# Performance work log

Measured on AMD Instinct MI355X. Metric: run time of the kernel, lower is better.

## Reference

```python
import jax, jax.numpy as jnp
import numpy as np

B, N, C_FEAT, FH, FW = 2, 6, 128, 28, 60
D, HEADS, DHEAD = 128, 4, 32
BH, BW = 32, 32
IMG_H, IMG_W = 224, 480
EPS = 1e-5

def _generate_grid(h, w):
    xs = np.linspace(0.0, 1.0, w, dtype=np.float32)
    ys = np.linspace(0.0, 1.0, h, dtype=np.float32)
    gx, gy = np.meshgrid(xs, ys, indexing='xy')  # (h, w)
    return np.stack([gx, gy, np.ones_like(gx)], 0)  # (3, h, w) homogeneous

def setup_inputs():
    key = jax.random.key(0)
    ks = iter(jax.random.split(key, 64))
    def nrm(shape, s=0.02):
        return jax.random.normal(next(ks), shape, dtype=jnp.float32) * s
    inp = {}
    inp['x'] = jax.random.normal(next(ks), (B, D, BH, BW), jnp.float32)
    inp['feature'] = jax.random.normal(next(ks), (B, N, C_FEAT, FH, FW), jnp.float32)
    inp['I_inv'] = jax.random.normal(next(ks), (B, N, 3, 3), jnp.float32)
    inp['E_inv'] = jax.random.normal(next(ks), (B, N, 4, 4), jnp.float32)
    inp['bev_grid'] = jax.random.uniform(next(ks), (3, BH, BW), jnp.float32) * 100.0
    plane = _generate_grid(FH, FW)
    plane[0] *= IMG_W
    plane[1] *= IMG_H
    inp['image_plane'] = jnp.asarray(plane)
    # feature_linear (fl) and feature_proj (fp): BN (eval) -> ReLU -> 1x1 conv
    for p in ('fl', 'fp'):
        inp[p + '_bn_g'] = jnp.ones((C_FEAT,), jnp.float32)
        inp[p + '_bn_b'] = jnp.zeros((C_FEAT,), jnp.float32)
        inp[p + '_bn_m'] = nrm((C_FEAT,), 0.1)
        inp[p + '_bn_v'] = jnp.ones((C_FEAT,), jnp.float32)
        inp[p + '_w'] = nrm((D, C_FEAT))
    inp['bev_w'] = nrm((D, 2)); inp['bev_b'] = nrm((D,))
    inp['img_w'] = nrm((D, 4)); inp['cam_w'] = nrm((D, 4))
    md = HEADS * DHEAD
    for p in ('q', 'k', 'v'):
        inp[p + '_ln_g'] = jnp.ones((D,), jnp.float32)
        inp[p + '_ln_b'] = jnp.zeros((D,), jnp.float32)
        inp[p + '_w'] = nrm((D, md))
        inp[p + '_b'] = nrm((md,))
    inp['proj_w'] = nrm((md, D)); inp['proj_b'] = nrm((D,))
    inp['pre_g'] = jnp.ones((D,), jnp.float32); inp['pre_b'] = jnp.zeros((D,), jnp.float32)
    inp['mlp_w1'] = nrm((D, 2 * D)); inp['mlp_b1'] = nrm((2 * D,))
    inp['mlp_w2'] = nrm((2 * D, D)); inp['mlp_b2'] = nrm((D,))
    inp['post_g'] = jnp.ones((D,), jnp.float32); inp['post_b'] = jnp.zeros((D,), jnp.float32)
    return inp

def _ln(t, g, b):
    mu = jnp.mean(t, -1, keepdims=True)
    var = jnp.mean((t - mu) ** 2, -1, keepdims=True)
    return (t - mu) * jax.lax.rsqrt(var + EPS) * g + b

def _bn_relu_conv(t, g, b, m, v, w):
    # eval-mode BatchNorm2d -> ReLU -> 1x1 conv (no bias); t: (B, C, H, W)
    th = (t - m[:, None, None]) * (g / jnp.sqrt(v + EPS))[:, None, None] + b[:, None, None]
    return jnp.einsum('oc,bchw->bohw', w, jax.nn.relu(th))

def reference(x, feature, I_inv, E_inv, bev_grid, image_plane,
              fl_bn_g, fl_bn_b, fl_bn_m, fl_bn_v, fl_w,
              fp_bn_g, fp_bn_b, fp_bn_m, fp_bn_v, fp_w,
              bev_w, bev_b, img_w, cam_w,
              q_ln_g, q_ln_b, q_w, q_b,
              k_ln_g, k_ln_b, k_w, k_b,
              v_ln_g, v_ln_b, v_w, v_b,
              proj_w, proj_b, pre_g, pre_b,
              mlp_w1, mlp_b1, mlp_w2, mlp_b2, post_g, post_b):
    b, n = feature.shape[:2]
    h, w = image_plane.shape[-2:]
    H, W = x.shape[-2:]
    dm = x.shape[1]
    # camera-center embedding: cam_embed 1x1 conv on translation column of E_inv
    c = E_inv[..., -1]                                             # (b, n, 4)
    c_embed = jnp.einsum('oc,bnc->bno', cam_w, c).reshape(b * n, dm)
    # per-pixel ray directions in world frame: d = E_inv @ pad(I_inv @ pixel, 1)
    pix = image_plane.reshape(3, h * w)
    cam = jnp.einsum('bnij,jk->bnik', I_inv, pix)                  # (b, n, 3, hw)
    cam = jnp.concatenate([cam, jnp.ones((b, n, 1, h * w), cam.dtype)], 2)
    d = jnp.einsum('bnij,bnjk->bnik', E_inv, cam)                  # (b, n, 4, hw)
    d_embed = jnp.einsum('oc,bnck->bnok', img_w, d).reshape(b * n, dm, h, w)
    img_embed = d_embed - c_embed[:, :, None, None]
    img_embed = img_embed / (jnp.linalg.norm(img_embed, axis=1, keepdims=True) + 1e-7)
    # bev positional embedding: bev_embed conv1x1 on world xy, minus camera embed
    w_embed = jnp.einsum('oc,chw->ohw', bev_w, bev_grid[:2]) + bev_b[:, None, None]
    bev_embed = w_embed[None] - c_embed[:, :, None, None]          # (bn, d, H, W)
    bev_embed = bev_embed / (jnp.linalg.norm(bev_embed, axis=1, keepdims=True) + 1e-7)
    query_pos = bev_embed.reshape(b, n, dm, H, W)
    feat_flat = feature.reshape(b * n, feature.shape[2], h, w)
    key_flat = img_embed + _bn_relu_conv(feat_flat, fp_bn_g, fp_bn_b, fp_bn_m, fp_bn_v, fp_w)
    val_flat = _bn_relu_conv(feat_flat, fl_bn_g, fl_bn_b, fl_bn_m, fl_bn_v, fl_w)
    query = query_pos + x[:, None]                                 # (b, n, d, H, W)
    # --- cross attention (softmax over all cameras' keys jointly) ---
    Q, K = H * W, h * w
    q = query.reshape(b, n, dm, Q).transpose(0, 1, 3, 2)           # (b, n, Q, d)
    k = key_flat.reshape(b, n, dm, K).transpose(0, 1, 3, 2)        # (b, n, K, d)
    v = val_flat.reshape(b, n, dm, K).transpose(0, 1, 3, 2).reshape(b, n * K, dm)
    q = _ln(q, q_ln_g, q_ln_b) @ q_w + q_b
    k = _ln(k, k_ln_g, k_ln_b) @ k_w + k_b
    v = _ln(v, v_ln_g, v_ln_b) @ v_w + v_b
    m, dh = HEADS, DHEAD
    qh = q.reshape(b, n, Q, m, dh)
    kh = k.reshape(b, n, K, m, dh)
    vh = v.reshape(b, n * K, m, dh)
    dot = (dh ** -0.5) * jnp.einsum('bnqmd,bnkmd->bmqnk', qh, kh)  # (b,m,Q,n,K)
    att = jax.nn.softmax(dot.reshape(b, m, Q, n * K), axis=-1)
    a = jnp.einsum('bmqK,bKmd->bqmd', att, vh).reshape(b, Q, m * dh)
    z = a @ proj_w + proj_b
    z = z + x.reshape(b, dm, Q).transpose(0, 2, 1)                 # skip connection
    z = _ln(z, pre_g, pre_b)
    z = z + (jax.nn.gelu(z @ mlp_w1 + mlp_b1, approximate=False) @ mlp_w2 + mlp_b2)
    z = _ln(z, post_g, post_b)
    return z.transpose(0, 2, 1).reshape(b, dm, H, W)
```

## Files before the change

### kernel.cpp

```cpp
#include <hip/hip_runtime.h>
#include <math.h>

#define EPSF 1e-5f

#define BB 2
#define NN 6
#define KPIX 1680
#define QQ 1024
#define SPLIT 6
#define KCHUNK (KPIX/SPLIT)
#define NPART (NN*SPLIT)
#define QKSCALE (0.17677669529663687f * 1.4426950408889634f)
#define NTILE_KV 53
#define KVGRID (BB*NN*NTILE_KV)

#define WOFF_FP   0
#define WOFF_FL   16384
#define WOFF_K    32768
#define WOFF_V    49152
#define WOFF_Q    65536
#define WOFF_PROJ 81920
#define WOFF_W1   98304
#define WOFF_W2   131072
#define WPK_ELEMS 163840

typedef __attribute__((ext_vector_type(8))) short bf16x8;
typedef __attribute__((ext_vector_type(16))) float f32x16;

__device__ __forceinline__ unsigned short f2bf(float f) {
  union { float f; unsigned u; } v; v.f = f;
  unsigned r = v.u + 0x7FFFu + ((v.u >> 16) & 1u);
  return (unsigned short)(r >> 16);
}
__device__ __forceinline__ float bf2f(unsigned short u) {
  union { unsigned u; float f; } v; v.u = ((unsigned)u) << 16; return v.f;
}
__device__ __forceinline__ unsigned pk_bf16(float lo, float hi) {
  unsigned r;
  asm volatile("v_cvt_pk_bf16_f32 %0, %1, %2" : "=v"(r) : "v"(lo), "v"(hi));
  return r;
}
__device__ __forceinline__ float fast_exp2(float x) {
  return __builtin_amdgcn_exp2f(x);
}
__device__ __forceinline__ void half_swap(unsigned &a, unsigned &b) {
#if __has_builtin(__builtin_amdgcn_permlane32_swap)
  auto r = __builtin_amdgcn_permlane32_swap(a, b, false, false);
  a = (unsigned)r[0]; b = (unsigned)r[1];
#else
  unsigned sa = (unsigned)__shfl_xor((int)a, 32);
  unsigned sb = (unsigned)__shfl_xor((int)b, 32);
  int hi = (threadIdx.x & 63) >> 5;
  unsigned na = hi ? sb : a;
  unsigned nb = hi ? b : sa;
  a = na; b = nb;
#endif
}

__global__ void pre_kernel(const float* __restrict__ fp_w, const float* __restrict__ fl_w,
                           const float* __restrict__ k_w, const float* __restrict__ v_w,
                           const float* __restrict__ q_w, const float* __restrict__ proj_w,
                           const float* __restrict__ mlp_w1, const float* __restrict__ mlp_w2,
                           const float* __restrict__ cam_w, const float* __restrict__ E_inv,
                           unsigned short* __restrict__ wp, float* __restrict__ c_embed) {
  int blk = blockIdx.x;
  int c = threadIdx.x;
  if (blk < 640) {
    int mat = blk >> 7, o = blk & 127;
    float v;
    if (mat == 0)      v = fp_w[o*128 + c];
    else if (mat == 1) v = fl_w[o*128 + c];
    else if (mat == 2) v = k_w[c*128 + o];
    else if (mat == 3) v = v_w[c*128 + o];
    else               v = q_w[c*128 + o] * QKSCALE;
    wp[(size_t)mat*16384 + o*128 + c] = f2bf(v);
  } else if (blk < 768) {
    int row = blk - 640;
    wp[WOFF_PROJ + row*128 + c] = f2bf(proj_w[c*128 + row]);
  } else if (blk < 1024) {
    int row = blk - 768;
    wp[WOFF_W1 + row*128 + c] = f2bf(mlp_w1[c*256 + row]);
  } else if (blk < 1280) {
    int i2 = blk - 1024;
    int row = i2 >> 1, col = (i2 & 1)*128 + c;
    wp[WOFF_W2 + row*256 + col] = f2bf(mlp_w2[col*128 + row]);
  } else {
    int bn = blk - 1280;
    const float* E = E_inv + bn * 16;
    float s = cam_w[c*4+0]*E[3] + cam_w[c*4+1]*E[7] + cam_w[c*4+2]*E[11] + cam_w[c*4+3]*E[15];
    c_embed[bn*128 + c] = s;
  }
}

__global__ __launch_bounds__(256) void proj_kernel(
    const float* __restrict__ feature, const float* __restrict__ I_inv,
    const float* __restrict__ E_inv, const float* __restrict__ image_plane,
    const float* __restrict__ c_embed, const float* __restrict__ img_w,
    const float* __restrict__ fp_bn_g, const float* __restrict__ fp_bn_b,
    const float* __restrict__ fp_bn_m, const float* __restrict__ fp_bn_v,
    const float* __restrict__ fl_bn_g, const float* __restrict__ fl_bn_b,
    const float* __restrict__ fl_bn_m, const float* __restrict__ fl_bn_v,
    const float* __restrict__ k_ln_g, const float* __restrict__ k_ln_b,
    const float* __restrict__ k_b,
    const float* __restrict__ v_ln_g, const float* __restrict__ v_ln_b,
    const float* __restrict__ v_b,
    const float* __restrict__ x, const float* __restrict__ bev_grid,
    const float* __restrict__ bev_w, const float* __restrict__ bev_b,
    const float* __restrict__ q_ln_g, const float* __restrict__ q_ln_b,
    const float* __restrict__ q_b,
    const unsigned short* __restrict__ wp,
    unsigned short* __restrict__ khb, unsigned short* __restrict__ vtb,
    unsigned short* __restrict__ qhb)
{
  __shared__ __align__(16) unsigned char smem[19456];
  int t = threadIdx.x;

  if (blockIdx.x < KVGRID) {
    unsigned short (*sA)[32*128] = reinterpret_cast<unsigned short(*)[32*128]>(smem);
    float (*sD)[32]     = reinterpret_cast<float(*)[32]>(smem + 16384);
    float (*sRed)[4][32] = reinterpret_cast<float(*)[4][32]>(smem + 16384 + 512);

    int blk = blockIdx.x;
    int bn = blk / NTILE_KV, tp = blk % NTILE_KV;
    int p0 = tp * 32;
    int wv = t >> 6, l = t & 63, lo = l & 31, hi = l >> 5;

    if (t < 32) {
      int pix = min(p0 + t, KPIX-1);
      const float* Ii = I_inv + bn*9;
      const float* Ei = E_inv + bn*16;
      float px = image_plane[pix], py = image_plane[KPIX + pix], pz = image_plane[2*KPIX + pix];
      float c0 = Ii[0]*px + Ii[1]*py + Ii[2]*pz;
      float c1 = Ii[3]*px + Ii[4]*py + Ii[5]*pz;
      float c2 = Ii[6]*px + Ii[7]*py + Ii[8]*pz;
      sD[0][t] = Ei[0]*c0 + Ei[1]*c1 + Ei[2]*c2  + Ei[3];
      sD[1][t] = Ei[4]*c0 + Ei[5]*c1 + Ei[6]*c2  + Ei[7];
      sD[2][t] = Ei[8]*c0 + Ei[9]*c1 + Ei[10]*c2 + Ei[11];
      sD[3][t] = Ei[12]*c0 + Ei[13]*c1 + Ei[14]*c2 + Ei[15];
    }

    {
      int path = t >> 7;
      int cp = (t >> 1) & 63;
      int ph = t & 1;
      int c0 = cp * 2;
      const float* bg = path ? fl_bn_g : fp_bn_g;
      const float* bb = path ? fl_bn_b : fp_bn_b;
      const float* bm = path ? fl_bn_m : fp_bn_m;
      const float* bv = path ? fl_bn_v : fp_bn_v;
      float g0 = bg[c0+0]*rsqrtf(bv[c0+0]+EPSF); float o0 = bb[c0+0] - bm[c0+0]*g0;
      float g1 = bg[c0+1]*rsqrtf(bv[c0+1]+EPSF); float o1 = bb[c0+1] - bm[c0+1]*g1;
      const float* frow0 = feature + ((size_t)bn*128 + c0)*KPIX;
      const float* frow1 = frow0 + KPIX;
#pragma unroll
      for (int i = 0; i < 4; ++i) {
        int plb = ph*16 + 4*i;
        int pix = p0 + plb;
        float4 f0, f1;
        if (pix + 3 < KPIX) {
          f0 = *(const float4*)(frow0 + pix);
          f1 = *(const float4*)(frow1 + pix);
        } else {
          f0.x = frow0[min(pix+0, KPIX-1)]; f0.y = frow0[min(pix+1, KPIX-1)];
          f0.z = frow0[min(pix+2, KPIX-1)]; f0.w = frow0[min(pix+3, KPIX-1)];
          f1.x = frow1[min(pix+0, KPIX-1)]; f1.y = frow1[min(pix+1, KPIX-1)];
          f1.z = frow1[min(pix+2, KPIX-1)]; f1.w = frow1[min(pix+3, KPIX-1)];
        }
        float fa[4] = {f0.x, f0.y, f0.z, f0.w};
        float fb[4] = {f1.x, f1.y, f1.z, f1.w};
#pragma unroll
        for (int j = 0; j < 4; ++j) {
          int pl = plb + j;
          int cc = c0 ^ ((pl & 7) << 3);
          ushort2 w;
          w.x = f2bf(fmaxf(fa[j]*g0 + o0, 0.f));
          w.y = f2bf(fmaxf(fb[j]*g1 + o1, 0.f));
          *(ushort2*)&sA[path][pl*128 + cc] = w;
        }
      }
    }
    __syncthreads();

    f32x16 acck = {}, accv = {};
    {
      const unsigned short* wfp = wp + WOFF_FP + (32*wv + lo)*128 + hi*8;
      const unsigned short* wfl = wp + WOFF_FL + (32*wv + lo)*128 + hi*8;
      int swz = (lo & 7) << 3;
#pragma unroll
      for (int s = 0; s < 8; ++s) {
        int cbase = s*16 + hi*8;
        bf16x8 a0 = *(const bf16x8*)(wfp + s*16);
        bf16x8 a1 = *(const bf16x8*)(wfl + s*16);
        bf16x8 b0 = *(const bf16x8*)&sA[0][lo*128 + (cbase ^ swz)];
        bf16x8 b1 = *(const bf16x8*)&sA[1][lo*128 + (cbase ^ swz)];
        acck = __builtin_amdgcn_mfma_f32_32x32x16_bf16(a0, b0, acck, 0, 0, 0);
        accv = __builtin_amdgcn_mfma_f32_32x32x16_bf16(a1, b1, accv, 0, 0, 0);
      }
    }

    float d0 = sD[0][lo], d1 = sD[1][lo], d2 = sD[2][lo], d3 = sD[3][lo];

    float ime[16];
    float ss = 0.f, vs1 = 0.f, vs2 = 0.f;
#pragma unroll
    for (int r = 0; r < 16; ++r) {
      int o = 32*wv + (r&3) + 8*(r>>2) + 4*hi;
      float4 iw = *(const float4*)(img_w + o*4);
      float de = iw.x*d0 + iw.y*d1 + iw.z*d2 + iw.w*d3 - c_embed[bn*128 + o];
      ime[r] = de; ss += de*de;
      float vv = accv[r];
      vs1 += vv; vs2 += vv*vv;
    }
    ss  += __shfl_xor(ss, 32);
    vs1 += __shfl_xor(vs1, 32);
    vs2 += __shfl_xor(vs2, 32);
    if (hi == 0) { sRed[0][wv][lo] = ss; sRed[1][wv][lo] = vs1; sRed[2][wv][lo] = vs2; }
    __syncthreads();
    float sst  = sRed[0][0][lo]+sRed[0][1][lo]+sRed[0][2][lo]+sRed[0][3][lo];
    float vs1t = sRed[1][0][lo]+sRed[1][1][lo]+sRed[1][2][lo]+sRed[1][3][lo];
    float vs2t = sRed[2][0][lo]+sRed[2][1][lo]+sRed[2][2][lo]+sRed[2][3][lo];
    float rinv = 1.f/(sqrtf(sst) + 1e-7f);
    float vmu = vs1t*(1.f/128.f);
    float vrs = rsqrtf(vs2t*(1.f/128.f) - vmu*vmu + EPSF);

    float kval[16];
    float ks1 = 0.f, ks2 = 0.f;
#pragma unroll
    for (int r = 0; r < 16; ++r) {
      float kv2 = acck[r] + ime[r]*rinv;
      kval[r] = kv2; ks1 += kv2; ks2 += kv2*kv2;
    }
    ks1 += __shfl_xor(ks1, 32);
    ks2 += __shfl_xor(ks2, 32);
    if (hi == 0) { sRed[3][wv][lo] = ks1; sRed[4][wv][lo] = ks2; }
    __syncthreads();
    float ks1t = sRed[3][0][lo]+sRed[3][1][lo]+sRed[3][2][lo]+sRed[3][3][lo];
    float ks2t = sRed[4][0][lo]+sRed[4][1][lo]+sRed[4][2][lo]+sRed[4][3][lo];
    float kmu = ks1t*(1.f/128.f);
    float krs = rsqrtf(ks2t*(1.f/128.f) - kmu*kmu + EPSF);

    {
      int swz = (lo & 7) << 3;
#pragma unroll
      for (int g = 0; g < 4; ++g) {
        int ob = 32*wv + 8*g + 4*hi;
        float4 kg = *(const float4*)(k_ln_g + ob);
        float4 kb2 = *(const float4*)(k_ln_b + ob);
        float4 vg = *(const float4*)(v_ln_g + ob);
        float4 vb2 = *(const float4*)(v_ln_b + ob);
        float kn0 = (kval[4*g+0]-kmu)*krs*kg.x + kb2.x;
        float kn1 = (kval[4*g+1]-kmu)*krs*kg.y + kb2.y;
        float kn2 = (kval[4*g+2]-kmu)*krs*kg.z + kb2.z;
        float kn3 = (kval[4*g+3]-kmu)*krs*kg.w + kb2.w;
        float vn0 = (accv[4*g+0]-vmu)*vrs*vg.x + vb2.x;
        float vn1 = (accv[4*g+1]-vmu)*vrs*vg.y + vb2.y;
        float vn2 = (accv[4*g+2]-vmu)*vrs*vg.z + vb2.z;
        float vn3 = (accv[4*g+3]-vmu)*vrs*vg.w + vb2.w;
        int idx = lo*128 + (ob ^ swz);
        *(ushort4*)&sA[0][idx] = make_ushort4(f2bf(kn0), f2bf(kn1), f2bf(kn2), f2bf(kn3));
        *(ushort4*)&sA[1][idx] = make_ushort4(f2bf(vn0), f2bf(vn1), f2bf(vn2), f2bf(vn3));
      }
    }
    __syncthreads();

    f32x16 a2k = {}, a2v = {};
    {
      const unsigned short* wk = wp + WOFF_K + (32*wv + lo)*128 + hi*8;
      const unsigned short* wv2 = wp + WOFF_V + (32*wv + lo)*128 + hi*8;
      int swz = (lo & 7) << 3;
#pragma unroll
      for (int s = 0; s < 8; ++s) {
        int cbase = s*16 + hi*8;
        bf16x8 a0 = *(const bf16x8*)(wk + s*16);
        bf16x8 a1 = *(const bf16x8*)(wv2 + s*16);
        bf16x8 b0 = *(const bf16x8*)&sA[0][lo*128 + (cbase ^ swz)];
        bf16x8 b1 = *(const bf16x8*)&sA[1][lo*128 + (cbase ^ swz)];
        a2k = __builtin_amdgcn_mfma_f32_32x32x16_bf16(a0, b0, a2k, 0, 0, 0);
        a2v = __builtin_amdgcn_mfma_f32_32x32x16_bf16(a1, b1, a2v, 0, 0, 0);
      }
    }

    int pix = p0 + lo;
    if (pix < KPIX) {
      unsigned short* krow = khb + ((size_t)bn*KPIX + pix)*128;
#pragma unroll
      for (int g = 0; g < 4; ++g) {
        int ob = 32*wv + 8*g + 4*hi;
        float4 kb4 = *(const float4*)(k_b + ob);
        *(ushort4*)(krow + ob) = make_ushort4(
          f2bf(a2k[4*g+0] + kb4.x), f2bf(a2k[4*g+1] + kb4.y),
          f2bf(a2k[4*g+2] + kb4.z), f2bf(a2k[4*g+3] + kb4.w));
        float4 vb4 = *(const float4*)(v_b + ob);
        vtb[((size_t)bn*128 + ob+0)*KPIX + pix] = f2bf(a2v[4*g+0] + vb4.x);
        vtb[((size_t)bn*128 + ob+1)*KPIX + pix] = f2bf(a2v[4*g+1] + vb4.y);
        vtb[((size_t)bn*128 + ob+2)*KPIX + pix] = f2bf(a2v[4*g+2] + vb4.z);
        vtb[((size_t)bn*128 + ob+3)*KPIX + pix] = f2bf(a2v[4*g+3] + vb4.w);
      }
    }
  } else {
    unsigned short* sQ = reinterpret_cast<unsigned short*>(smem);
    float (*sRedQ)[8][32] = reinterpret_cast<float(*)[8][32]>(smem + 8192);

    int qblk = blockIdx.x - KVGRID;
    int bn = qblk >> 5, qt = qblk & 31;
    int p0 = qt * 32;
    int b = bn / NN;

    {
      int q = t & 31, og = t >> 5;
      int qi = p0 + q;
      float gx = bev_grid[qi], gy = bev_grid[QQ + qi];
      float be[16]; float ss = 0.f;
#pragma unroll
      for (int j = 0; j < 16; ++j) {
        int o = og*16 + j;
        float we = bev_w[o*2+0]*gx + bev_w[o*2+1]*gy + bev_b[o];
        float v = we - c_embed[bn*128 + o];
        be[j] = v; ss += v*v;
      }
      sRedQ[0][og][q] = ss;
      __syncthreads();
      float sst = 0.f;
#pragma unroll
      for (int g = 0; g < 8; ++g) sst += sRedQ[0][g][q];
      float rinv = 1.f/(sqrtf(sst) + 1e-7f);
      float s1 = 0.f, s2 = 0.f;
#pragma unroll
      for (int j = 0; j < 16; ++j) {
        int o = og*16 + j;
        float qv = be[j]*rinv + x[((size_t)(b*128 + o))*QQ + qi];
        be[j] = qv; s1 += qv; s2 += qv*qv;
      }
      sRedQ[1][og][q] = s1; sRedQ[2][og][q] = s2;
      __syncthreads();
      float s1t = 0.f, s2t = 0.f;
#pragma unroll
      for (int g = 0; g < 8; ++g) { s1t += sRedQ[1][g][q]; s2t += sRedQ[2][g][q]; }
      float mu = s1t*(1.f/128.f);
      float rs = rsqrtf(s2t*(1.f/128.f) - mu*mu + EPSF);
      int swz = (q & 7) << 3;
#pragma unroll
      for (int u = 0; u < 4; ++u) {
        int ob = og*16 + 4*u;
        float4 qg = *(const float4*)(q_ln_g + ob);
        float4 qb2 = *(const float4*)(q_ln_b + ob);
        *(ushort4*)&sQ[q*128 + (ob ^ swz)] = make_ushort4(
          f2bf((be[4*u+0]-mu)*rs*qg.x + qb2.x), f2bf((be[4*u+1]-mu)*rs*qg.y + qb2.y),
          f2bf((be[4*u+2]-mu)*rs*qg.z + qb2.z), f2bf((be[4*u+3]-mu)*rs*qg.w + qb2.w));
      }
    }
    __syncthreads();

    {
      int wvv = t >> 6, l = t & 63, lo = l & 31, hi = l >> 5;
      const unsigned short* wq = wp + WOFF_Q + (32*wvv + lo)*128 + hi*8;
      int swz = (lo & 7) << 3;
      f32x16 acc = {};
#pragma unroll
      for (int s = 0; s < 8; ++s) {
        int cbase = s*16 + hi*8;
        bf16x8 a0 = *(const bf16x8*)(wq + s*16);
        bf16x8 b0 = *(const bf16x8*)&sQ[lo*128 + (cbase ^ swz)];
        acc = __builtin_amdgcn_mfma_f32_32x32x16_bf16(a0, b0, acc, 0, 0, 0);
      }
      unsigned short* qrow = qhb + ((size_t)bn*QQ + p0 + lo)*128;
#pragma unroll
      for (int g = 0; g < 4; ++g) {
        int ob = 32*wvv + 8*g + 4*hi;
        float4 qb4 = *(const float4*)(q_b + ob);
        *(ushort4*)(qrow + ob) = make_ushort4(
          f2bf(acc[4*g+0] + qb4.x*QKSCALE), f2bf(acc[4*g+1] + qb4.y*QKSCALE),
          f2bf(acc[4*g+2] + qb4.z*QKSCALE), f2bf(acc[4*g+3] + qb4.w*QKSCALE));
      }
    }
  }
}

__global__ __launch_bounds__(256) void attn_kernel(
    const unsigned short* __restrict__ qhb, const unsigned short* __restrict__ khb,
    const unsigned short* __restrict__ vtb,
    float* __restrict__ lsum, unsigned short* __restrict__ pacb)
{
  int blk = blockIdx.x;
  int sp = blk % SPLIT; blk /= SPLIT;
  int n  = blk % NN;    blk /= NN;
  int qt = blk % 16;    blk /= 16;
  int b  = blk;
  int t = threadIdx.x;
  int wave = t >> 6, l = t & 63, lo = l & 31, hi = l >> 5;
  int dho = wave * 32;
  int bn = b*NN + n;

  bf16x8 qf[2][2];
#pragma unroll
  for (int g = 0; g < 2; ++g) {
    const unsigned short* qrow = qhb + ((size_t)bn*QQ + qt*64 + g*32 + lo)*128 + dho + hi*8;
    qf[g][0] = *(const bf16x8*)(qrow);
    qf[g][1] = *(const bf16x8*)(qrow + 16);
  }

  f32x16 acc[2] = {};
  float lr[2] = {0.f, 0.f};

  int k0 = sp * KCHUNK, kend = k0 + KCHUNK;
  int kfull_end = k0 + (KCHUNK & ~31);
  const unsigned short* kbase = khb + (size_t)bn*KPIX*128 + dho + hi*8;
  const unsigned short* vrow  = vtb + ((size_t)bn*128 + dho + lo)*KPIX;

  bf16x8 kf0, kf1, vf0, vf1;
  {
    const unsigned short* krow = kbase + (size_t)(k0 + lo)*128;
    kf0 = *(const bf16x8*)(krow);
    kf1 = *(const bf16x8*)(krow + 16);
    vf0 = *(const bf16x8*)(vrow + k0 + hi*8);
    vf1 = *(const bf16x8*)(vrow + k0 + 16 + hi*8);
  }

  for (int K0 = k0; K0 < kfull_end; K0 += 32) {
    int Kn = K0 + 32;
    const unsigned short* krow = kbase + (size_t)(Kn + lo)*128;
    bf16x8 nk0 = *(const bf16x8*)(krow);
    bf16x8 nk1 = *(const bf16x8*)(krow + 16);
    bf16x8 nv0 = *(const bf16x8*)(vrow + Kn + hi*8);
    bf16x8 nv1 = *(const bf16x8*)(vrow + Kn + 16 + hi*8);

#pragma unroll
    for (int g = 0; g < 2; ++g) {
      f32x16 s = {};
      __builtin_amdgcn_s_setprio(1);
      s = __builtin_amdgcn_mfma_f32_32x32x16_bf16(kf0, qf[g][0], s, 0, 0, 0);
      s = __builtin_amdgcn_mfma_f32_32x32x16_bf16(kf1, qf[g][1], s, 0, 0, 0);
      __builtin_amdgcn_s_setprio(0);
      float p[16];
      float lsub = 0.f;
#pragma unroll
      for (int r = 0; r < 16; ++r) { float e = fast_exp2(s[r]); p[r] = e; lsub += e; }
      lr[g] += lsub;
#pragma unroll
      for (int ks = 0; ks < 2; ++ks) {
        int rb = ks*8;
        unsigned a0 = pk_bf16(p[rb+0], p[rb+1]);
        unsigned c0 = pk_bf16(p[rb+2], p[rb+3]);
        unsigned b0 = pk_bf16(p[rb+4], p[rb+5]);
        unsigned d0 = pk_bf16(p[rb+6], p[rb+7]);
        half_swap(a0, b0);
        half_swap(c0, d0);
        union { unsigned u[4]; bf16x8 v; } pa;
        pa.u[0] = a0; pa.u[1] = c0; pa.u[2] = b0; pa.u[3] = d0;
        __builtin_amdgcn_s_setprio(1);
        acc[g] = __builtin_amdgcn_mfma_f32_32x32x16_bf16(pa.v, ks ? vf1 : vf0, acc[g], 0, 0, 0);
        __builtin_amdgcn_s_setprio(0);
      }
    }
    kf0 = nk0; kf1 = nk1; vf0 = nv0; vf1 = nv1;
  }

  {
    int K0 = kfull_end;
#pragma unroll
    for (int g = 0; g < 2; ++g) {
      f32x16 s = {};
      __builtin_amdgcn_s_setprio(1);
      s = __builtin_amdgcn_mfma_f32_32x32x16_bf16(kf0, qf[g][0], s, 0, 0, 0);
      s = __builtin_amdgcn_mfma_f32_32x32x16_bf16(kf1, qf[g][1], s, 0, 0, 0);
      __builtin_amdgcn_s_setprio(0);
      float p[16];
      float lsub = 0.f;
#pragma unroll
      for (int r = 0; r < 16; ++r) {
        int key = K0 + (r&3) + 8*(r>>2) + 4*hi;
        float e = (key < kend) ? fast_exp2(s[r]) : 0.f;
        p[r] = e; lsub += e;
      }
      lr[g] += lsub;
#pragma unroll
      for (int ks = 0; ks < 2; ++ks) {
        int rb = ks*8;
        unsigned a0 = pk_bf16(p[rb+0], p[rb+1]);
        unsigned c0 = pk_bf16(p[rb+2], p[rb+3]);
        unsigned b0 = pk_bf16(p[rb+4], p[rb+5]);
        unsigned d0 = pk_bf16(p[rb+6], p[rb+7]);
        half_swap(a0, b0);
        half_swap(c0, d0);
        union { unsigned u[4]; bf16x8 v; } pa;
        pa.u[0] = a0; pa.u[1] = c0; pa.u[2] = b0; pa.u[3] = d0;
        __builtin_amdgcn_s_setprio(1);
        acc[g] = __builtin_amdgcn_mfma_f32_32x32x16_bf16(pa.v, ks ? vf1 : vf0, acc[g], 0, 0, 0);
        __builtin_amdgcn_s_setprio(0);
      }
    }
  }

  size_t hb = ((size_t)(b*4 + wave)*NPART + (n*SPLIT + sp))*QQ;
#pragma unroll
  for (int g = 0; g < 2; ++g) {
    float ltot = lr[g] + __shfl_xor(lr[g], 32);
    if (hi == 0) lsum[hb + qt*64 + g*32 + lo] = ltot;
#pragma unroll
    for (int r = 0; r < 16; ++r) {
      int crow = (r&3) + 8*(r>>2) + 4*hi;
      pacb[(hb + qt*64 + g*32 + crow)*32 + lo] = f2bf(acc[g][r]);
    }
  }
}

__global__ __launch_bounds__(512) void epi_kernel(
    const float* __restrict__ lsum, const unsigned short* __restrict__ pacb,
    const float* __restrict__ x, const unsigned short* __restrict__ wp,
    const float* __restrict__ proj_b,
    const float* __restrict__ pre_g, const float* __restrict__ pre_b,
    const float* __restrict__ mlp_b1, const float* __restrict__ mlp_b2,
    const float* __restrict__ post_g, const float* __restrict__ post_b,
    float* __restrict__ out)
{
  int blk = blockIdx.x;
  int b = blk >> 5, qt = blk & 31;
  int q0 = qt * 32;
  int t = threadIdx.x;
  int wv = t >> 6, l = t & 63, lo = l & 31, hi = l >> 5;
  int rt = wv & 3, kh = wv >> 2;

  __shared__ unsigned short sA[32*128];
  __shared__ unsigned short sZ[32*128];
  __shared__ unsigned short sH[32*256];
  __shared__ float sPar[4][64][16];
  __shared__ float sRedE[2][4][32];

  {
    int q = t & 31, g = t >> 5;
    int m = g >> 2, dl = (g & 3) * 8;
    size_t basehm = ((size_t)(b*4 + m)*NPART)*QQ + q0 + q;
    float lt = 0.f;
    float av[8] = {0,0,0,0,0,0,0,0};
    for (int j = 0; j < NPART; ++j) {
      size_t base = basehm + (size_t)j*QQ;
      lt += lsum[base];
      const unsigned short* pp = pacb + base*32 + dl;
      ushort4 u0 = *(const ushort4*)(pp);
      ushort4 u1 = *(const ushort4*)(pp + 4);
      av[0] += bf2f(u0.x); av[1] += bf2f(u0.y); av[2] += bf2f(u0.z); av[3] += bf2f(u0.w);
      av[4] += bf2f(u1.x); av[5] += bf2f(u1.y); av[6] += bf2f(u1.z); av[7] += bf2f(u1.w);
    }
    float rl = 1.f / lt;
    int swz = (q & 7) << 3;
    int dg = (g*8) ^ swz;
    *(ushort4*)&sA[q*128 + dg] = make_ushort4(
      f2bf(av[0]*rl), f2bf(av[1]*rl), f2bf(av[2]*rl), f2bf(av[3]*rl));
    *(ushort4*)&sA[q*128 + dg + 4] = make_ushort4(
      f2bf(av[4]*rl), f2bf(av[5]*rl), f2bf(av[6]*rl), f2bf(av[7]*rl));
  }
  __syncthreads();

  f32x16 acc = {};
  {
    const unsigned short* wA = wp + WOFF_PROJ + (32*rt + lo)*128 + kh*64 + hi*8;
    int swz = (lo & 7) << 3;
#pragma unroll
    for (int s = 0; s < 4; ++s) {
      int cb = kh*64 + s*16 + hi*8;
      bf16x8 a0 = *(const bf16x8*)(wA + s*16);
      bf16x8 b0 = *(const bf16x8*)&sA[lo*128 + (cb ^ swz)];
      acc = __builtin_amdgcn_mfma_f32_32x32x16_bf16(a0, b0, acc, 0, 0, 0);
    }
  }
  if (wv >= 4) {
#pragma unroll
    for (int r = 0; r < 16; ++r) sPar[wv-4][l][r] = acc[r];
  }
  __syncthreads();

  float znr[16], zv[16];
  if (wv < 4) {
    float s1 = 0.f, s2 = 0.f;
#pragma unroll
    for (int r = 0; r < 16; ++r) {
      int o = 32*rt + (r&3) + 8*(r>>2) + 4*hi;
      float z = acc[r] + sPar[wv][l][r] + proj_b[o] + x[((size_t)b*128 + o)*QQ + q0 + lo];
      zv[r] = z; s1 += z; s2 += z*z;
    }
    s1 += __shfl_xor(s1, 32); s2 += __shfl_xor(s2, 32);
    if (hi == 0) { sRedE[0][rt][lo] = s1; sRedE[1][rt][lo] = s2; }
  }
  __syncthreads();
  if (wv < 4) {
    float s1t = sRedE[0][0][lo]+sRedE[0][1][lo]+sRedE[0][2][lo]+sRedE[0][3][lo];
    float s2t = sRedE[1][0][lo]+sRedE[1][1][lo]+sRedE[1][2][lo]+sRedE[1][3][lo];
    float mu = s1t*(1.f/128.f);
    float rs = rsqrtf(s2t*(1.f/128.f) - mu*mu + EPSF);
    int swz = (lo & 7) << 3;
#pragma unroll
    for (int g2 = 0; g2 < 4; ++g2) {
      int ob = 32*rt + 8*g2 + 4*hi;
      float4 pg = *(const float4*)(pre_g + ob);
      float4 pb = *(const float4*)(pre_b + ob);
      float z0 = (zv[4*g2+0]-mu)*rs*pg.x + pb.x;
      float z1 = (zv[4*g2+1]-mu)*rs*pg.y + pb.y;
      float z2 = (zv[4*g2+2]-mu)*rs*pg.z + pb.z;
      float z3 = (zv[4*g2+3]-mu)*rs*pg.w + pb.w;
      znr[4*g2+0] = z0; znr[4*g2+1] = z1; znr[4*g2+2] = z2; znr[4*g2+3] = z3;
      *(ushort4*)&sZ[lo*128 + (ob ^ swz)] = make_ushort4(f2bf(z0), f2bf(z1), f2bf(z2), f2bf(z3));
    }
  }
  __syncthreads();

  {
    f32x16 acch = {};
    const unsigned short* wA = wp + WOFF_W1 + (32*wv + lo)*128 + hi*8;
    int swz = (lo & 7) << 3;
#pragma unroll
    for (int s = 0; s < 8; ++s) {
      int cb = s*16 + hi*8;
      bf16x8 a0 = *(const bf16x8*)(wA + s*16);
      bf16x8 b0 = *(const bf16x8*)&sZ[lo*128 + (cb ^ swz)];
      acch = __builtin_amdgcn_mfma_f32_32x32x16_bf16(a0, b0, acch, 0, 0, 0);
    }
#pragma unroll
    for (int g2 = 0; g2 < 4; ++g2) {
      int hrow = 32*wv + 8*g2 + 4*hi;
      float4 b1 = *(const float4*)(mlp_b1 + hrow);
      float h0 = acch[4*g2+0] + b1.x, h1 = acch[4*g2+1] + b1.y;
      float h2 = acch[4*g2+2] + b1.z, h3 = acch[4*g2+3] + b1.w;
      float g0 = 0.5f*h0*(1.f + erff(h0*0.7071067811865476f));
      float g1 = 0.5f*h1*(1.f + erff(h1*0.7071067811865476f));
      float g2f = 0.5f*h2*(1.f + erff(h2*0.7071067811865476f));
      float g3 = 0.5f*h3*(1.f + erff(h3*0.7071067811865476f));
      *(ushort4*)&sH[lo*256 + (hrow ^ swz)] = make_ushort4(f2bf(g0), f2bf(g1), f2bf(g2f), f2bf(g3));
    }
  }
  __syncthreads();

  f32x16 acc2 = {};
  {
    const unsigned short* wA = wp + WOFF_W2 + (32*rt + lo)*256 + kh*128 + hi*8;
    int swz = (lo & 7) << 3;
#pragma unroll
    for (int s = 0; s < 8; ++s) {
      int cb = kh*128 + s*16 + hi*8;
      bf16x8 a0 = *(const bf16x8*)(wA + s*16);
      bf16x8 b0 = *(const bf16x8*)&sH[lo*256 + (cb ^ swz)];
      acc2 = __builtin_amdgcn_mfma_f32_32x32x16_bf16(a0, b0, acc2, 0, 0, 0);
    }
  }
  if (wv >= 4) {
#pragma unroll
    for (int r = 0; r < 16; ++r) sPar[wv-4][l][r] = acc2[r];
  }
  __syncthreads();

  float z2v[16];
  if (wv < 4) {
    float s1 = 0.f, s2 = 0.f;
#pragma unroll
    for (int r = 0; r < 16; ++r) {
      int o = 32*rt + (r&3) + 8*(r>>2) + 4*hi;
      float z2 = znr[r] + acc2[r] + sPar[wv][l][r] + mlp_b2[o];
      z2v[r] = z2; s1 += z2; s2 += z2*z2;
    }
    s1 += __shfl_xor(s1, 32); s2 += __shfl_xor(s2, 32);
    if (hi == 0) { sRedE[0][rt][lo] = s1; sRedE[1][rt][lo] = s2; }
  }
  __syncthreads();
  if (wv < 4) {
    float s1t = sRedE[0][0][lo]+sRedE[0][1][lo]+sRedE[0][2][lo]+sRedE[0][3][lo];
    float s2t = sRedE[1][0][lo]+sRedE[1][1][lo]+sRedE[1][2][lo]+sRedE[1][3][lo];
    float mu = s1t*(1.f/128.f);
    float rs = rsqrtf(s2t*(1.f/128.f) - mu*mu + EPSF);
#pragma unroll
    for (int r = 0; r < 16; ++r) {
      int o = 32*rt + (r&3) + 8*(r>>2) + 4*hi;
      out[((size_t)b*128 + o)*QQ + q0 + lo] = (z2v[r]-mu)*rs*post_g[o] + post_b[o];
    }
  }
}

extern "C" void kernel_launch(void* const* d_in, const int* in_sizes, int n_in,
                              void* d_out, int out_size, void* d_ws, size_t ws_size,
                              hipStream_t stream) {
  const float* x           = (const float*)d_in[0];
  const float* feature     = (const float*)d_in[1];
  const float* I_inv       = (const float*)d_in[2];
  const float* E_inv       = (const float*)d_in[3];
  const float* bev_grid    = (const float*)d_in[4];
  const float* image_plane = (const float*)d_in[5];
  const float* fl_bn_g = (const float*)d_in[6];
  const float* fl_bn_b = (const float*)d_in[7];
  const float* fl_bn_m = (const float*)d_in[8];
  const float* fl_bn_v = (const float*)d_in[9];
  const float* fl_w    = (const float*)d_in[10];
  const float* fp_bn_g = (const float*)d_in[11];
  const float* fp_bn_b = (const float*)d_in[12];
  const float* fp_bn_m = (const float*)d_in[13];
  const float* fp_bn_v = (const float*)d_in[14];
  const float* fp_w    = (const float*)d_in[15];
  const float* bev_w   = (const float*)d_in[16];
  const float* bev_b   = (const float*)d_in[17];
  const float* img_w   = (const float*)d_in[18];
  const float* cam_w   = (const float*)d_in[19];
  const float* q_ln_g  = (const float*)d_in[20];
  const float* q_ln_b  = (const float*)d_in[21];
  const float* q_w     = (const float*)d_in[22];
  const float* q_b     = (const float*)d_in[23];
  const float* k_ln_g  = (const float*)d_in[24];
  const float* k_ln_b  = (const float*)d_in[25];
  const float* k_w     = (const float*)d_in[26];
  const float* k_b     = (const float*)d_in[27];
  const float* v_ln_g  = (const float*)d_in[28];
  const float* v_ln_b  = (const float*)d_in[29];
  const float* v_w     = (const float*)d_in[30];
  const float* v_b     = (const float*)d_in[31];
  const float* proj_w  = (const float*)d_in[32];
  const float* proj_b  = (const float*)d_in[33];
  const float* pre_g   = (const float*)d_in[34];
  const float* pre_b   = (const float*)d_in[35];
  const float* mlp_w1  = (const float*)d_in[36];
  const float* mlp_b1  = (const float*)d_in[37];
  const float* mlp_w2  = (const float*)d_in[38];
  const float* mlp_b2  = (const float*)d_in[39];
  const float* post_g  = (const float*)d_in[40];
  const float* post_b  = (const float*)d_in[41];

  float* ws = (float*)d_ws;
  float* c_embed = ws;
  float* lsum = ws + 1536;
  unsigned short* pacb = (unsigned short*)(lsum + (size_t)BB*4*NPART*QQ);
  unsigned short* qhb = pacb + (size_t)BB*4*NPART*QQ*32;
  unsigned short* khb = qhb + (size_t)BB*NN*QQ*128;
  unsigned short* vtb = khb + (size_t)BB*NN*KPIX*128;
  unsigned short* wpk = vtb + (size_t)BB*NN*KPIX*128;
  float* out = (float*)d_out;

  hipLaunchKernelGGL(pre_kernel, dim3(1280 + BB*NN), dim3(128), 0, stream,
                     fp_w, fl_w, k_w, v_w, q_w, proj_w, mlp_w1, mlp_w2,
                     cam_w, E_inv, wpk, c_embed);
  hipLaunchKernelGGL(proj_kernel, dim3(KVGRID + BB*NN*32), dim3(256), 0, stream,
                     feature, I_inv, E_inv, image_plane, c_embed, img_w,
                     fp_bn_g, fp_bn_b, fp_bn_m, fp_bn_v,
                     fl_bn_g, fl_bn_b, fl_bn_m, fl_bn_v,
                     k_ln_g, k_ln_b, k_b,
                     v_ln_g, v_ln_b, v_b,
                     x, bev_grid, bev_w, bev_b,
                     q_ln_g, q_ln_b, q_b,
                     wpk, khb, vtb, qhb);
  hipLaunchKernelGGL(attn_kernel, dim3(BB*16*NN*SPLIT), dim3(256), 0, stream,
                     qhb, khb, vtb, lsum, pacb);
  hipLaunchKernelGGL(epi_kernel, dim3(BB*32), dim3(512), 0, stream,
                     lsum, pacb, x, wpk, proj_b, pre_g, pre_b,
                     mlp_b1, mlp_b2, post_g, post_b, out);
}
```

Measured before the change: 87.45 us.

## Fully unroll attention key loop in pairs and precompute KV embed norm before sync

The attention kernel's key loop now handles two 32-key tiles per step. Their QK MFMAs are interleaved, the loop is fully unrolled over the fixed chunk length of 280 keys, and the next 64 keys are prefetched. This adds instruction-level parallelism and removes loop overhead. The KV projection kernel now computes the image-embedding squared norm per pixel across all threads before the first barrier, which removes one __syncthreads and one reduction round. The cost is more register pressure from the doubled fragments, plus redundant recomputation of the camera-direction math in every thread.

```diff
diff --git a/kernel.cpp b/kernel.cpp
--- a/kernel.cpp
+++ b/kernel.cpp
@@ -112,13 +112,14 @@
     unsigned short* __restrict__ khb, unsigned short* __restrict__ vtb,
     unsigned short* __restrict__ qhb)
 {
-  __shared__ __align__(16) unsigned char smem[19456];
+  __shared__ __align__(16) unsigned char smem[19968];
   int t = threadIdx.x;
 
   if (blockIdx.x < KVGRID) {
     unsigned short (*sA)[32*128] = reinterpret_cast<unsigned short(*)[32*128]>(smem);
-    float (*sD)[32]     = reinterpret_cast<float(*)[32]>(smem + 16384);
+    float (*sD)[32]      = reinterpret_cast<float(*)[32]>(smem + 16384);
     float (*sRed)[4][32] = reinterpret_cast<float(*)[4][32]>(smem + 16384 + 512);
+    float (*sSS)[32]     = reinterpret_cast<float(*)[32]>(smem + 16384 + 512 + 2048);
 
     int blk = blockIdx.x;
     int bn = blk / NTILE_KV, tp = blk % NTILE_KV;
@@ -179,6 +180,30 @@
         }
       }
     }
+
+    {
+      int pxl = t & 31, og = t >> 5;
+      int pix = min(p0 + pxl, KPIX-1);
+      const float* Ii = I_inv + bn*9;
+      const float* Ei = E_inv + bn*16;
+      float px = image_plane[pix], py = image_plane[KPIX + pix], pz = image_plane[2*KPIX + pix];
+      float c0 = Ii[0]*px + Ii[1]*py + Ii[2]*pz;
+      float c1 = Ii[3]*px + Ii[4]*py + Ii[5]*pz;
+      float c2 = Ii[6]*px + Ii[7]*py + Ii[8]*pz;
+      float d0 = Ei[0]*c0 + Ei[1]*c1 + Ei[2]*c2  + Ei[3];
+      float d1 = Ei[4]*c0 + Ei[5]*c1 + Ei[6]*c2  + Ei[7];
+      float d2 = Ei[8]*c0 + Ei[9]*c1 + Ei[10]*c2 + Ei[11];
+      float d3 = Ei[12]*c0 + Ei[13]*c1 + Ei[14]*c2 + Ei[15];
+      float ssp = 0.f;
+#pragma unroll
+      for (int j = 0; j < 16; ++j) {
+        int o = og*16 + j;
+        float4 iw = *(const float4*)(img_w + o*4);
+        float de = iw.x*d0 + iw.y*d1 + iw.z*d2 + iw.w*d3 - c_embed[bn*128 + o];
+        ssp += de*de;
+      }
+      sSS[og][pxl] = ssp;
+    }
     __syncthreads();
 
     f32x16 acck = {}, accv = {};
@@ -198,46 +223,37 @@
       }
     }
 
+    float sst = sSS[0][lo]+sSS[1][lo]+sSS[2][lo]+sSS[3][lo]
+              + sSS[4][lo]+sSS[5][lo]+sSS[6][lo]+sSS[7][lo];
+    float rinv = 1.f/(sqrtf(sst) + 1e-7f);
     float d0 = sD[0][lo], d1 = sD[1][lo], d2 = sD[2][lo], d3 = sD[3][lo];
 
-    float ime[16];
-    float ss = 0.f, vs1 = 0.f, vs2 = 0.f;
+    float kval[16];
+    float ks1 = 0.f, ks2 = 0.f, vs1 = 0.f, vs2 = 0.f;
 #pragma unroll
     for (int r = 0; r < 16; ++r) {
       int o = 32*wv + (r&3) + 8*(r>>2) + 4*hi;
       float4 iw = *(const float4*)(img_w + o*4);
       float de = iw.x*d0 + iw.y*d1 + iw.z*d2 + iw.w*d3 - c_embed[bn*128 + o];
-      ime[r] = de; ss += de*de;
-      float vv = accv[r];
-      vs1 += vv; vs2 += vv*vv;
-    }
-    ss  += __shfl_xor(ss, 32);
-    vs1 += __shfl_xor(vs1, 32);
-    vs2 += __shfl_xor(vs2, 32);
-    if (hi == 0) { sRed[0][wv][lo] = ss; sRed[1][wv][lo] = vs1; sRed[2][wv][lo] = vs2; }
+      float kv2 = acck[r] + de*rinv;
+      kval[r] = kv2; ks1 += kv2; ks2 += kv2*kv2;
+      float vv = accv[r]; vs1 += vv; vs2 += vv*vv;
+    }
+    ks1 += __shfl_xor(ks1, 32); ks2 += __shfl_xor(ks2, 32);
+    vs1 += __shfl_xor(vs1, 32); vs2 += __shfl_xor(vs2, 32);
+    if (hi == 0) {
+      sRed[0][wv][lo] = ks1; sRed[1][wv][lo] = ks2;
+      sRed[2][wv][lo] = vs1; sRed[3][wv][lo] = vs2;
+    }
     __syncthreads();
-    float sst  = sRed[0][0][lo]+sRed[0][1][lo]+sRed[0][2][lo]+sRed[0][3][lo];
-    float vs1t = sRed[1][0][lo]+sRed[1][1][lo]+sRed[1][2][lo]+sRed[1][3][lo];
-    float vs2t = sRed[2][0][lo]+sRed[2][1][lo]+sRed[2][2][lo]+sRed[2][3][lo];
-    float rinv = 1.f/(sqrtf(sst) + 1e-7f);
+    float ks1t = sRed[0][0][lo]+sRed[0][1][lo]+sRed[0][2][lo]+sRed[0][3][lo];
+    float ks2t = sRed[1][0][lo]+sRed[1][1][lo]+sRed[1][2][lo]+sRed[1][3][lo];
+    float vs1t = sRed[2][0][lo]+sRed[2][1][lo]+sRed[2][2][lo]+sRed[2][3][lo];
+    float vs2t = sRed[3][0][lo]+sRed[3][1][lo]+sRed[3][2][lo]+sRed[3][3][lo];
+    float kmu = ks1t*(1.f/128.f);
+    float krs = rsqrtf(ks2t*(1.f/128.f) - kmu*kmu + EPSF);
     float vmu = vs1t*(1.f/128.f);
     float vrs = rsqrtf(vs2t*(1.f/128.f) - vmu*vmu + EPSF);
-
-    float kval[16];
-    float ks1 = 0.f, ks2 = 0.f;
-#pragma unroll
-    for (int r = 0; r < 16; ++r) {
-      float kv2 = acck[r] + ime[r]*rinv;
-      kval[r] = kv2; ks1 += kv2; ks2 += kv2*kv2;
-    }
-    ks1 += __shfl_xor(ks1, 32);
-    ks2 += __shfl_xor(ks2, 32);
-    if (hi == 0) { sRed[3][wv][lo] = ks1; sRed[4][wv][lo] = ks2; }
-    __syncthreads();
-    float ks1t = sRed[3][0][lo]+sRed[3][1][lo]+sRed[3][2][lo]+sRed[3][3][lo];
-    float ks2t = sRed[4][0][lo]+sRed[4][1][lo]+sRed[4][2][lo]+sRed[4][3][lo];
-    float kmu = ks1t*(1.f/128.f);
-    float krs = rsqrtf(ks2t*(1.f/128.f) - kmu*kmu + EPSF);
 
     {
       int swz = (lo & 7) << 3;
@@ -403,38 +419,111 @@
   float lr[2] = {0.f, 0.f};
 
   int k0 = sp * KCHUNK, kend = k0 + KCHUNK;
-  int kfull_end = k0 + (KCHUNK & ~31);
   const unsigned short* kbase = khb + (size_t)bn*KPIX*128 + dho + hi*8;
   const unsigned short* vrow  = vtb + ((size_t)bn*128 + dho + lo)*KPIX;
 
-  bf16x8 kf0, kf1, vf0, vf1;
+  bf16x8 kA0, kA1, vA0, vA1, kB0, kB1, vB0, vB1;
   {
-    const unsigned short* krow = kbase + (size_t)(k0 + lo)*128;
-    kf0 = *(const bf16x8*)(krow);
-    kf1 = *(const bf16x8*)(krow + 16);
-    vf0 = *(const bf16x8*)(vrow + k0 + hi*8);
-    vf1 = *(const bf16x8*)(vrow + k0 + 16 + hi*8);
-  }
-
-  for (int K0 = k0; K0 < kfull_end; K0 += 32) {
-    int Kn = K0 + 32;
-    const unsigned short* krow = kbase + (size_t)(Kn + lo)*128;
-    bf16x8 nk0 = *(const bf16x8*)(krow);
-    bf16x8 nk1 = *(const bf16x8*)(krow + 16);
-    bf16x8 nv0 = *(const bf16x8*)(vrow + Kn + hi*8);
-    bf16x8 nv1 = *(const bf16x8*)(vrow + Kn + 16 + hi*8);
-
+    const unsigned short* kr = kbase + (size_t)(k0 + lo)*128;
+    kA0 = *(const bf16x8*)(kr); kA1 = *(const bf16x8*)(kr + 16);
+    vA0 = *(const bf16x8*)(vrow + k0 + hi*8);
+    vA1 = *(const bf16x8*)(vrow + k0 + 16 + hi*8);
+    kr = kbase + (size_t)(k0 + 32 + lo)*128;
+    kB0 = *(const bf16x8*)(kr); kB1 = *(const bf16x8*)(kr + 16);
+    vB0 = *(const bf16x8*)(vrow + k0 + 32 + hi*8);
+    vB1 = *(const bf16x8*)(vrow + k0 + 32 + 16 + hi*8);
+  }
+
+#pragma unroll
+  for (int it = 0; it < 4; ++it) {
+    int K0 = k0 + it*64;
+    bf16x8 nA0, nA1, nvA0, nvA1, nB0, nB1, nvB0, nvB1;
+    {
+      int Kn = K0 + 64;
+      const unsigned short* kr = kbase + (size_t)(Kn + lo)*128;
+      nA0 = *(const bf16x8*)(kr); nA1 = *(const bf16x8*)(kr + 16);
+      nvA0 = *(const bf16x8*)(vrow + Kn + hi*8);
+      nvA1 = *(const bf16x8*)(vrow + Kn + 16 + hi*8);
+      if (it < 3) {
+        kr = kbase + (size_t)(Kn + 32 + lo)*128;
+        nB0 = *(const bf16x8*)(kr); nB1 = *(const bf16x8*)(kr + 16);
+        nvB0 = *(const bf16x8*)(vrow + Kn + 32 + hi*8);
+        nvB1 = *(const bf16x8*)(vrow + Kn + 32 + 16 + hi*8);
+      } else {
+        nB0 = nA0; nB1 = nA1; nvB0 = nvA0; nvB1 = nvA1;
+      }
+    }
+
+#pragma unroll
+    for (int g = 0; g < 2; ++g) {
+      f32x16 sA_ = {}, sB_ = {};
+      __builtin_amdgcn_s_setprio(1);
+      sA_ = __builtin_amdgcn_mfma_f32_32x32x16_bf16(kA0, qf[g][0], sA_, 0, 0, 0);
+      sB_ = __builtin_amdgcn_mfma_f32_32x32x16_bf16(kB0, qf[g][0], sB_, 0, 0, 0);
+      sA_ = __builtin_amdgcn_mfma_f32_32x32x16_bf16(kA1, qf[g][1], sA_, 0, 0, 0);
+      sB_ = __builtin_amdgcn_mfma_f32_32x32x16_bf16(kB1, qf[g][1], sB_, 0, 0, 0);
+      __builtin_amdgcn_s_setprio(0);
+      float pA[16], pB[16];
+      float lsub = 0.f;
+#pragma unroll
+      for (int r = 0; r < 16; ++r) {
+        float eA = fast_exp2(sA_[r]); pA[r] = eA;
+        float eB = fast_exp2(sB_[r]); pB[r] = eB;
+        lsub += eA + eB;
+      }
+      lr[g] += lsub;
+#pragma unroll
+      for (int ks = 0; ks < 2; ++ks) {
+        int rb = ks*8;
+        unsigned a0 = pk_bf16(pA[rb+0], pA[rb+1]);
+        unsigned c0 = pk_bf16(pA[rb+2], pA[rb+3]);
+        unsigned b0 = pk_bf16(pA[rb+4], pA[rb+5]);
+        unsigned d0 = pk_bf16(pA[rb+6], pA[rb+7]);
+        half_swap(a0, b0);
+        half_swap(c0, d0);
+        union { unsigned u[4]; bf16x8 v; } pa;
+        pa.u[0] = a0; pa.u[1] = c0; pa.u[2] = b0; pa.u[3] = d0;
+        __builtin_amdgcn_s_setprio(1);
+        acc[g] = __builtin_amdgcn_mfma_f32_32x32x16_bf16(pa.v, ks ? vA1 : vA0, acc[g], 0, 0, 0);
+        __builtin_amdgcn_s_setprio(0);
+      }
+#pragma unroll
+      for (int ks = 0; ks < 2; ++ks) {
+        int rb = ks*8;
+        unsigned a0 = pk_bf16(pB[rb+0], pB[rb+1]);
+        unsigned c0 = pk_bf16(pB[rb+2], pB[rb+3]);
+        unsigned b0 = pk_bf16(pB[rb+4], pB[rb+5]);
+        unsigned d0 = pk_bf16(pB[rb+6], pB[rb+7]);
+        half_swap(a0, b0);
+        half_swap(c0, d0);
+        union { unsigned u[4]; bf16x8 v; } pa;
+        pa.u[0] = a0; pa.u[1] = c0; pa.u[2] = b0; pa.u[3] = d0;
+        __builtin_amdgcn_s_setprio(1);
+        acc[g] = __builtin_amdgcn_mfma_f32_32x32x16_bf16(pa.v, ks ? vB1 : vB0, acc[g], 0, 0, 0);
+        __builtin_amdgcn_s_setprio(0);
+      }
+    }
+    kA0 = nA0; kA1 = nA1; vA0 = nvA0; vA1 = nvA1;
+    kB0 = nB0; kB1 = nB1; vB0 = nvB0; vB1 = nvB1;
+  }
+
+  {
+    int K0 = k0 + 256;
 #pragma unroll
     for (int g = 0; g < 2; ++g) {
       f32x16 s = {};
       __builtin_amdgcn_s_setprio(1);
-      s = __builtin_amdgcn_mfma_f32_32x32x16_bf16(kf0, qf[g][0], s, 0, 0, 0);
-      s = __builtin_amdgcn_mfma_f32_32x32x16_bf16(kf1, qf[g][1], s, 0, 0, 0);
+      s = __builtin_amdgcn_mfma_f32_32x32x16_bf16(kA0, qf[g][0], s, 0, 0, 0);
+      s = __builtin_amdgcn_mfma_f32_32x32x16_bf16(kA1, qf[g][1], s, 0, 0, 0);
       __builtin_amdgcn_s_setprio(0);
       float p[16];
       float lsub = 0.f;
 #pragma unroll
-      for (int r = 0; r < 16; ++r) { float e = fast_exp2(s[r]); p[r] = e; lsub += e; }
+      for (int r = 0; r < 16; ++r) {
+        int key = K0 + (r&3) + 8*(r>>2) + 4*hi;
+        float e = (key < kend) ? fast_exp2(s[r]) : 0.f;
+        p[r] = e; lsub += e;
+      }
       lr[g] += lsub;
 #pragma unroll
       for (int ks = 0; ks < 2; ++ks) {
@@ -448,44 +537,7 @@
         union { unsigned u[4]; bf16x8 v; } pa;
         pa.u[0] = a0; pa.u[1] = c0; pa.u[2] = b0; pa.u[3] = d0;
         __builtin_amdgcn_s_setprio(1);
-        acc[g] = __builtin_amdgcn_mfma_f32_32x32x16_bf16(pa.v, ks ? vf1 : vf0, acc[g], 0, 0, 0);
-        __builtin_amdgcn_s_setprio(0);
-      }
-    }
-    kf0 = nk0; kf1 = nk1; vf0 = nv0; vf1 = nv1;
-  }
-
-  {
-    int K0 = kfull_end;
-#pragma unroll
-    for (int g = 0; g < 2; ++g) {
-      f32x16 s = {};
-      __builtin_amdgcn_s_setprio(1);
-      s = __builtin_amdgcn_mfma_f32_32x32x16_bf16(kf0, qf[g][0], s, 0, 0, 0);
-      s = __builtin_amdgcn_mfma_f32_32x32x16_bf16(kf1, qf[g][1], s, 0, 0, 0);
-      __builtin_amdgcn_s_setprio(0);
-      float p[16];
-      float lsub = 0.f;
-#pragma unroll
-      for (int r = 0; r < 16; ++r) {
-        int key = K0 + (r&3) + 8*(r>>2) + 4*hi;
-        float e = (key < kend) ? fast_exp2(s[r]) : 0.f;
-        p[r] = e; lsub += e;
-      }
-      lr[g] += lsub;
-#pragma unroll
-      for (int ks = 0; ks < 2; ++ks) {
-        int rb = ks*8;
-        unsigned a0 = pk_bf16(p[rb+0], p[rb+1]);
-        unsigned c0 = pk_bf16(p[rb+2], p[rb+3]);
-        unsigned b0 = pk_bf16(p[rb+4], p[rb+5]);
-        unsigned d0 = pk_bf16(p[rb+6], p[rb+7]);
-        half_swap(a0, b0);
-        half_swap(c0, d0);
-        union { unsigned u[4]; bf16x8 v; } pa;
-        pa.u[0] = a0; pa.u[1] = c0; pa.u[2] = b0; pa.u[3] = d0;
-        __builtin_amdgcn_s_setprio(1);
-        acc[g] = __builtin_amdgcn_mfma_f32_32x32x16_bf16(pa.v, ks ? vf1 : vf0, acc[g], 0, 0, 0);
+        acc[g] = __builtin_amdgcn_mfma_f32_32x32x16_bf16(pa.v, ks ? vA1 : vA0, acc[g], 0, 0, 0);
         __builtin_amdgcn_s_setprio(0);
       }
     }
```

Measured after the change: 93.80 us. 1.07x slower.
